# Kernel optimization log

Measured on AMD Instinct MI355X. Metric: run time of the kernel, lower is better.

Reference implementation:

```python
import jax, jax.numpy as jnp
import numpy as np
import math

B, S, E, H = 2, 2048, 1024, 8
Dh = E // H  # 128


def setup_inputs() -> dict:
    key = jax.random.key(0)
    ks = jax.random.split(key, 9)
    g = lambda k, shp: jax.random.normal(k, shp, jnp.float32) * 0.02
    return {
        "inputs": jax.random.normal(ks[0], (B, S, E), jnp.float32),
        "ln_gamma": jnp.ones((E,), jnp.float32),
        "ln_beta": jnp.zeros((E,), jnp.float32),
        "Wq": g(ks[1], (Dh, Dh)), "bq": jnp.zeros((Dh,), jnp.float32),
        "Wk": g(ks[2], (Dh, Dh)), "bk": jnp.zeros((Dh,), jnp.float32),
        "Wv": g(ks[3], (Dh, Dh)), "bv": jnp.zeros((Dh,), jnp.float32),
        "Wp": g(ks[4], (Dh, Dh)),  # pos_proj has no bias
        "u_bias": g(ks[5], (H, Dh)),
        "v_bias": g(ks[6], (H, Dh)),
        "Wo": g(ks[7], (E, E)), "bo": jnp.zeros((E,), jnp.float32),
    }


def _pos_encoding(s, e):
    # sinusoidal PE, interleaved sin/cos as in the torch module
    pos = jnp.arange(s, dtype=jnp.float32)[:, None]
    div = jnp.exp(jnp.arange(0, e, 2, dtype=jnp.float32) * (-math.log(10000.0) / e))
    pe = jnp.zeros((s, e), jnp.float32)
    pe = pe.at[:, 0::2].set(jnp.sin(pos * div))
    pe = pe.at[:, 1::2].set(jnp.cos(pos * div))
    return pe


def _rel_shift(ps):
    # Transformer-XL relative shift: pad a zero column, reshape, drop first row
    b, h, s1, s2 = ps.shape
    padded = jnp.pad(ps, ((0, 0), (0, 0), (0, 0), (1, 0)))
    return padded.reshape(b, h, s2 + 1, s1)[:, :, 1:, :].reshape(b, h, s1, s2)


def _forward(inputs, ln_gamma, ln_beta, Wq, bq, Wk, bk, Wv, bv, Wp, u_bias, v_bias, Wo, bo):
    b, s, e = inputs.shape
    # LayerNorm (biased variance, eps=1e-5 like nn.LayerNorm)
    mu = inputs.mean(-1, keepdims=True)
    var = inputs.var(-1, keepdims=True)
    xn = (inputs - mu) / jnp.sqrt(var + 1e-5) * ln_gamma + ln_beta

    xh = xn.reshape(b, s, H, Dh)              # split heads before per-head Dh x Dh projections
    q = xh @ Wq + bq                           # (b, s, H, Dh)
    k = xh @ Wk + bk
    v = xh @ Wv + bv

    pe = _pos_encoding(s, e).reshape(s, H, Dh)  # same for every batch element
    p = pe @ Wp                                 # (s, H, Dh)

    content = jnp.einsum('bqhd,bkhd->bhqk', q + u_bias, k)
    pos_score = jnp.einsum('bqhd,khd->bhqk', q + v_bias, p)
    pos_score = _rel_shift(pos_score)
    score = (content + pos_score) / jnp.sqrt(jnp.float32(e))  # note: scales by sqrt(embed_dim), faithful to source

    attn = jax.nn.softmax(score, axis=-1)
    ctx = jnp.einsum('bhqk,bkhd->bqhd', attn, v).reshape(b, s, e)
    # dropout is identity at inference
    return ctx @ Wo + bo


def reference(inputs, ln_gamma, ln_beta, Wq, bq, Wk, bk, Wv, bv, Wp, u_bias, v_bias, Wo, bo):
    return _forward(inputs, ln_gamma, ln_beta, Wq, bq, Wk, bk, Wv, bv, Wp, u_bias, v_bias, Wo, bo)
```

## Files before the change

kernel.cpp:

```cpp
#include <hip/hip_runtime.h>
#include <hip/hip_bf16.h>

#define SDIM 2048
#define EDIM 1024

typedef __attribute__((ext_vector_type(8))) short bf16x8;
typedef __attribute__((ext_vector_type(4))) short bf16x4;
typedef __attribute__((ext_vector_type(4))) float f32x4;
typedef __hip_bfloat16 bf16;

#define MFMA(a, b, c) __builtin_amdgcn_mfma_f32_16x16x32_bf16((a), (b), (c), 0, 0, 0)

#define GLDS16(g, l)                                                      \
  __builtin_amdgcn_global_load_lds(                                       \
      (const __attribute__((address_space(1))) unsigned int*)(g),         \
      (__attribute__((address_space(3))) unsigned int*)(l), 16, 0, 0)

__device__ __forceinline__ bf16x8 ld8(const bf16* p) {
  return *(const bf16x8*)p;
}
__device__ __forceinline__ float b2f(short s) {
  union { float f; unsigned u; } v; v.u = ((unsigned)(unsigned short)s) << 16; return v.f;
}

__device__ __forceinline__ void wcast_body(const float* __restrict__ w, bf16* __restrict__ wt,
                                           int blk, int R, int C) {
  __shared__ float tile[32][33];
  int cb = C >> 5;
  int br = blk / cb, bc = blk % cb;
  int r0 = br << 5, c0 = bc << 5;
  int tr = threadIdx.x >> 5, tc = threadIdx.x & 31;
#pragma unroll
  for (int i = 0; i < 32; i += 8)
    tile[tr + i][tc] = w[(size_t)(r0 + tr + i) * C + c0 + tc];
  __syncthreads();
#pragma unroll
  for (int i = 0; i < 32; i += 8)
    wt[(size_t)(c0 + tr + i) * R + r0 + tc] = __float2bfloat16(tile[tc][tr + i]);
}

__global__ __launch_bounds__(256) void wcast_all(const float* __restrict__ wo, const float* __restrict__ w0,
                                                 const float* __restrict__ w1, const float* __restrict__ w2,
                                                 const float* __restrict__ w3, bf16* __restrict__ oo,
                                                 bf16* __restrict__ o0, bf16* __restrict__ o1,
                                                 bf16* __restrict__ o2, bf16* __restrict__ o3) {
  int blk = blockIdx.x;
  if (blk < 1024) {
    wcast_body(wo, oo, blk, 1024, 1024);
  } else {
    int which = (blk - 1024) >> 4;
    const float* w = which == 0 ? w0 : which == 1 ? w1 : which == 2 ? w2 : w3;
    bf16* o = which == 0 ? o0 : which == 1 ? o1 : which == 2 ? o2 : o3;
    wcast_body(w, o, (blk - 1024) & 15, 128, 128);
  }
}

__global__ __launch_bounds__(256) void ln_kernel(const float* __restrict__ x, const float* __restrict__ g,
                                                 const float* __restrict__ be, bf16* __restrict__ xn) {
  int tok = blockIdx.x;
  const float4 v = ((const float4*)(x + (size_t)tok * EDIM))[threadIdx.x];
  float s = v.x + v.y + v.z + v.w;
  float s2 = v.x * v.x + v.y * v.y + v.z * v.z + v.w * v.w;
#pragma unroll
  for (int o = 1; o < 64; o <<= 1) { s += __shfl_xor(s, o); s2 += __shfl_xor(s2, o); }
  __shared__ float ls[8];
  if ((threadIdx.x & 63) == 0) { ls[threadIdx.x >> 6] = s; ls[4 + (threadIdx.x >> 6)] = s2; }
  __syncthreads();
  s = ls[0] + ls[1] + ls[2] + ls[3];
  s2 = ls[4] + ls[5] + ls[6] + ls[7];
  float mu = s * (1.0f / EDIM);
  float rstd = rsqrtf(s2 * (1.0f / EDIM) - mu * mu + 1e-5f);
  int c = threadIdx.x * 4;
  const float4 gv = ((const float4*)g)[threadIdx.x];
  const float4 bv = ((const float4*)be)[threadIdx.x];
  bf16* o = xn + (size_t)tok * EDIM + c;
  o[0] = __float2bfloat16((v.x - mu) * rstd * gv.x + bv.x);
  o[1] = __float2bfloat16((v.y - mu) * rstd * gv.y + bv.y);
  o[2] = __float2bfloat16((v.z - mu) * rstd * gv.z + bv.z);
  o[3] = __float2bfloat16((v.w - mu) * rstd * gv.w + bv.w);
}

__global__ __launch_bounds__(256) void pe_kernel(bf16* __restrict__ pe) {
  int s = blockIdx.x;
  for (int i = threadIdx.x; i < EDIM / 2; i += 256) {
    float div = __expf((float)(2 * i) * (-9.210340371976184f / (float)EDIM));
    float a = (float)s * div;
    float sv, cv;
    sincosf(a, &sv, &cv);
    pe[(size_t)s * EDIM + 2 * i] = __float2bfloat16(sv);
    pe[(size_t)s * EDIM + 2 * i + 1] = __float2bfloat16(cv);
  }
}

template <int MODE>
__device__ __forceinline__ void proj_body(const bf16* __restrict__ A, const bf16* __restrict__ WT,
                                          const float* __restrict__ bias, const float* __restrict__ ubias,
                                          const float* __restrict__ vbias, bf16* __restrict__ out0,
                                          bf16* __restrict__ out1, int blk, bf16* tl) {
  const int row0 = blk * 128;
  const int lane = threadIdx.x & 63, wid = threadIdx.x >> 6;
  const int wr = (wid >> 1) * 64, wc = (wid & 1) * 64;
  const int lg = lane >> 4, lr = lane & 15;
  f32x4 acc[4][4] = {};
#pragma unroll
  for (int kf = 0; kf < 4; ++kf) {
    const int k0 = kf * 32 + lg * 8;
    bf16x8 a[4], b[4];
#pragma unroll
    for (int m = 0; m < 4; ++m) a[m] = ld8(A + (size_t)(row0 + wr + m * 16 + lr) * 128 + k0);
#pragma unroll
    for (int n = 0; n < 4; ++n) b[n] = ld8(WT + (size_t)(wc + n * 16 + lr) * 128 + k0);
#pragma unroll
    for (int m = 0; m < 4; ++m)
#pragma unroll
      for (int n = 0; n < 4; ++n) acc[m][n] = MFMA(a[m], b[n], acc[m][n]);
  }
  if constexpr (MODE == 2) {
#pragma unroll
    for (int m = 0; m < 4; ++m)
#pragma unroll
      for (int n = 0; n < 4; ++n) {
        int col = wc + n * 16 + lr;
#pragma unroll
        for (int r = 0; r < 4; ++r) {
          int lrow = wr + m * 16 + lg * 4 + r;
          tl[col * 132 + lrow] = __float2bfloat16(acc[m][n][r] + bias[col]);
        }
      }
    __syncthreads();
    int tok0 = row0 >> 3;
    int b = tok0 >> 11, s0 = tok0 & 2047;
#pragma unroll
    for (int i = 0; i < 4; ++i) {
      int pair = threadIdx.x + 256 * i;
      int h = pair >> 7, d = pair & 127;
      bf16 tmp[16];
#pragma unroll
      for (int j = 0; j < 16; ++j) tmp[j] = tl[d * 132 + j * 8 + h];
      size_t o = ((size_t)((b * 8 + h) * 128 + d)) * SDIM + s0;
      *(bf16x8*)(out0 + o) = *(bf16x8*)(&tmp[0]);
      *(bf16x8*)(out0 + o + 8) = *(bf16x8*)(&tmp[8]);
    }
  } else {
#pragma unroll
    for (int m = 0; m < 4; ++m)
#pragma unroll
      for (int n = 0; n < 4; ++n) {
        int col = wc + n * 16 + lr;
#pragma unroll
        for (int r = 0; r < 4; ++r) {
          int row = row0 + wr + m * 16 + lg * 4 + r;
          float val = acc[m][n][r];
          if constexpr (MODE == 0) {
            int h = row & 7, tok = row >> 3;
            int b = tok >> 11, s = tok & 2047;
            size_t o = ((size_t)((b * 8 + h) * SDIM + s)) * 128 + col;
            val += bias[col];
            out0[o] = __float2bfloat16((val + ubias[h * 128 + col]) * 0.03125f);
            out1[o] = __float2bfloat16((val + vbias[h * 128 + col]) * 0.03125f);
          } else if constexpr (MODE == 1) {
            int h = row & 7, tok = row >> 3;
            int b = tok >> 11, s = tok & 2047;
            out0[((size_t)((b * 8 + h) * SDIM + s)) * 128 + col] = __float2bfloat16(val + bias[col]);
          } else {
            int h = row & 7, s = row >> 3;
            out0[((size_t)(h * SDIM + s)) * 128 + col] = __float2bfloat16(val);
          }
        }
      }
  }
}

__global__ __launch_bounds__(256) void proj_all(const bf16* __restrict__ xn, const bf16* __restrict__ peb,
                                                const bf16* __restrict__ wqt, const bf16* __restrict__ wkt,
                                                const bf16* __restrict__ wvt, const bf16* __restrict__ wpt,
                                                const float* __restrict__ bq, const float* __restrict__ bk,
                                                const float* __restrict__ bv, const float* __restrict__ ub,
                                                const float* __restrict__ vbias, bf16* __restrict__ qub,
                                                bf16* __restrict__ qvb, bf16* __restrict__ kbb,
                                                bf16* __restrict__ vtb, bf16* __restrict__ pb) {
  __shared__ bf16 tl[128 * 132];
  int blk = blockIdx.x;
  if (blk < 256) proj_body<0>(xn, wqt, bq, ub, vbias, qub, qvb, blk, tl);
  else if (blk < 512) proj_body<1>(xn, wkt, bk, nullptr, nullptr, kbb, nullptr, blk - 256, tl);
  else if (blk < 768) proj_body<2>(xn, wvt, bv, nullptr, nullptr, vtb, nullptr, blk - 512, tl);
  else proj_body<3>(peb, wpt, nullptr, nullptr, nullptr, pb, nullptr, blk - 768, tl);
}

__global__ __launch_bounds__(256) void ps_kernel(const bf16* __restrict__ qv, const bf16* __restrict__ p,
                                                 bf16* __restrict__ ps) {
  const int bh = blockIdx.x & 15;
  const int t = blockIdx.x >> 4;
  const int q0 = (t >> 4) * 128, j0 = (t & 15) * 128;
  const int h = bh & 7;
  const bf16* Aq = qv + (size_t)bh * SDIM * 128;
  const bf16* Ph = p + (size_t)h * SDIM * 128;
  const int lane = threadIdx.x & 63, wid = threadIdx.x >> 6;
  const int wr = (wid >> 1) * 64, wc = (wid & 1) * 64;
  const int lg = lane >> 4, lr = lane & 15;
  f32x4 acc[4][4] = {};
#pragma unroll
  for (int kf = 0; kf < 4; ++kf) {
    const int k0 = kf * 32 + lg * 8;
    bf16x8 a[4], b[4];
#pragma unroll
    for (int m = 0; m < 4; ++m) a[m] = ld8(Aq + (size_t)(q0 + wr + m * 16 + lr) * 128 + k0);
#pragma unroll
    for (int n = 0; n < 4; ++n) b[n] = ld8(Ph + (size_t)(j0 + wc + n * 16 + lr) * 128 + k0);
#pragma unroll
    for (int m = 0; m < 4; ++m)
#pragma unroll
      for (int n = 0; n < 4; ++n) acc[m][n] = MFMA(a[m], b[n], acc[m][n]);
  }
  __shared__ bf16 tl[128 * 136];
#pragma unroll
  for (int m = 0; m < 4; ++m)
#pragma unroll
    for (int n = 0; n < 4; ++n) {
      int jl = wc + n * 16 + lr;
#pragma unroll
      for (int r = 0; r < 4; ++r) {
        int ql = wr + m * 16 + lg * 4 + r;
        tl[ql * 136 + jl] = __float2bfloat16(acc[m][n][r]);
      }
    }
  __syncthreads();
  bf16* po = ps + (size_t)bh * SDIM * SDIM + (size_t)q0 * SDIM + j0;
#pragma unroll
  for (int i = 0; i < 8; ++i) {
    int id = threadIdx.x + 256 * i;
    int row = id >> 4, seg = id & 15;
    bf16x8 v = *(const bf16x8*)(tl + row * 136 + seg * 8);
    *(bf16x8*)(po + (size_t)row * SDIM + seg * 8) = v;
  }
}

#define PSLOAD(KT, WLO, WHI)                                              \
  {                                                                       \
    _Pragma("unroll")                                                     \
    for (int nf = 0; nf < 4; ++nf) {                                      \
      const int K0 = (KT) + nf * 16 + lg * 4;                             \
      const bool a_ = (K0 + 3 <= Q);                                      \
      const bf16* wp = a_ ? (pA + K0 - padA) : (pB + K0 - padB);          \
      WLO[nf] = *(const unsigned long long*)wp;                           \
      WHI[nf] = *(const unsigned long long*)(wp + 4);                     \
    }                                                                     \
  }

#define STAGE(KT, BUF)                                                    \
  {                                                                       \
    _Pragma("unroll")                                                     \
    for (int i = 0; i < 4; ++i) {                                         \
      int rb = wid * 16 + i * 4;                                          \
      int row = rb + krow_l;                                              \
      GLDS16(Kp + (size_t)((KT) + row) * 128 + ((kc16 ^ (row & 7)) << 3), \
             &kl[BUF][rb * 128]);                                         \
    }                                                                     \
    _Pragma("unroll")                                                     \
    for (int i = 0; i < 4; ++i) {                                         \
      int rb = wid * 32 + i * 8;                                          \
      int d = rb + vrow_l;                                                \
      GLDS16(Vp + (size_t)d * SDIM + (KT) + ((vc8 ^ (d & 7)) << 3),       \
             &vl[BUF][rb * 64]);                                          \
    }                                                                     \
  }

#define TILE(KT, BUF, WLO, WHI, VMSTR)                                    \
  {                                                                       \
    asm volatile("s_waitcnt vmcnt(" VMSTR ")" ::: "memory");              \
    __builtin_amdgcn_s_barrier();                                         \
    __builtin_amdgcn_sched_barrier(0);                                    \
    const bf16* klc = &kl[BUF][0];                                        \
    const bf16* vlc = &vl[BUF][0];                                        \
    f32x4 sc[4] = {};                                                     \
    _Pragma("unroll")                                                     \
    for (int nf = 0; nf < 4; ++nf) {                                      \
      const int krow = nf * 16 + lr;                                      \
      const bf16* kr = klc + krow * 128;                                  \
      const int sw = (krow & 7) << 3;                                     \
      _Pragma("unroll")                                                   \
      for (int kf = 0; kf < 4; ++kf) {                                    \
        bf16x8 kfrag = *(const bf16x8*)(kr + (((kf * 4 + lg) << 3) ^ sw));\
        sc[nf] = MFMA(kfrag, qfr[kf], sc[nf]);                            \
      }                                                                   \
    }                                                                     \
    bf16x4 pscur[4];                                                      \
    _Pragma("unroll")                                                     \
    for (int nf = 0; nf < 4; ++nf) {                                      \
      const int K0 = (KT) + nf * 16 + lg * 4;                             \
      const bool a_ = (K0 + 3 <= Q);                                      \
      const bool bp = (K0 >= Q + 2);                                      \
      const int sh = (a_ ? padA : padB) << 4;                             \
      unsigned long long w =                                              \
          sh ? ((WLO[nf] >> sh) | (WHI[nf] << (64 - sh))) : WLO[nf];      \
      union { unsigned long long u; bf16x4 v; } cv;                       \
      cv.u = w;                                                           \
      bf16x4 pv = cv.v;                                                   \
      if (!a_ && !bp) {                                                   \
        _Pragma("unroll")                                                 \
        for (int r = 0; r < 4; ++r) {                                     \
          const int K = K0 + r;                                           \
          if (K <= Q) pv[r] = ((const short*)pA)[K];                      \
          else if (K == Q + 1) pv[r] = (short)0;                          \
        }                                                                 \
      }                                                                   \
      pscur[nf] = pv;                                                     \
    }                                                                     \
    _Pragma("unroll")                                                     \
    for (int nf = 0; nf < 4; ++nf) {                                      \
      float e0 = __expf(sc[nf][0] + b2f(pscur[nf][0]));                   \
      float e1 = __expf(sc[nf][1] + b2f(pscur[nf][1]));                   \
      float e2 = __expf(sc[nf][2] + b2f(pscur[nf][2]));                   \
      float e3 = __expf(sc[nf][3] + b2f(pscur[nf][3]));                   \
      rsum += (e0 + e1) + (e2 + e3);                                      \
      bf16 tmp[4] = {__float2bfloat16(e0), __float2bfloat16(e1),          \
                     __float2bfloat16(e2), __float2bfloat16(e3)};         \
      *(bf16x4*)(plw + lr * 72 + nf * 16 + lg * 4) = *(bf16x4*)tmp;       \
    }                                                                     \
    bf16x8 pa[2];                                                         \
    _Pragma("unroll")                                                     \
    for (int k2 = 0; k2 < 2; ++k2)                                        \
      pa[k2] = *(const bf16x8*)(plw + lr * 72 + k2 * 32 + lg * 8);        \
    _Pragma("unroll")                                                     \
    for (int nf = 0; nf < 8; ++nf) {                                      \
      const int d = nf * 16 + lr;                                         \
      const bf16* vr = vlc + d * 64;                                      \
      const int swd = (d & 7) << 3;                                       \
      _Pragma("unroll")                                                   \
      for (int k2 = 0; k2 < 2; ++k2) {                                    \
        bf16x8 vb = *(const bf16x8*)(vr + (((k2 * 4 + lg) << 3) ^ swd));  \
        cacc[nf] = MFMA(pa[k2], vb, cacc[nf]);                            \
      }                                                                   \
    }                                                                     \
    asm volatile("" ::: "memory");                                        \
    __builtin_amdgcn_s_barrier();                                         \
    __builtin_amdgcn_sched_barrier(0);                                    \
  }

__global__ __launch_bounds__(256) void attn_kernel(const bf16* __restrict__ qu, const bf16* __restrict__ kb,
                                                   const bf16* __restrict__ vt, const bf16* __restrict__ ps,
                                                   bf16* __restrict__ ctx) {
  const int bh = blockIdx.x & 15, qblk = blockIdx.x >> 4;
  const int b = bh >> 3, h = bh & 7;
  const int lane = threadIdx.x & 63, wid = threadIdx.x >> 6;
  const int lg = lane >> 4, lr = lane & 15;
  const int q0 = qblk * 64 + wid * 16;
  const bf16* Kp = kb + (size_t)bh * SDIM * 128;
  const bf16* Vp = vt + (size_t)bh * 128 * SDIM;

  const bf16* psbh = ps + (size_t)bh * SDIM * SDIM;
  const int Q = q0 + lr;
  const bf16* pA = psbh + (size_t)(Q + 1) * (SDIM - 1);
  const bf16* pB = psbh + (size_t)(Q + 1) * SDIM - Q - 2;
  const int padA = (int)(((unsigned)(Q + 1) * (SDIM - 1)) & 3);
  const int padB = (int)(((unsigned)(Q + 1) * SDIM - Q - 2) & 3);

  __shared__ bf16 kl[2][64 * 128];
  __shared__ bf16 vl[2][128 * 64];
  __shared__ bf16 pl[4][16 * 72];
  bf16* plw = &pl[wid][0];

  const int krow_l = lane >> 4, kc16 = lane & 15;
  const int vrow_l = lane >> 3, vc8 = lane & 7;

  bf16x8 qfr[4];
#pragma unroll
  for (int kf = 0; kf < 4; ++kf)
    qfr[kf] = ld8(qu + (size_t)bh * SDIM * 128 + (size_t)(q0 + lr) * 128 + kf * 32 + lg * 8);

  f32x4 cacc[8] = {};
  float rsum = 0.f;

  unsigned long long wloA[4], whiA[4], wloB[4], whiB[4];

  PSLOAD(0, wloA, whiA);
  STAGE(0, 0);
  PSLOAD(64, wloB, whiB);
  STAGE(64, 1);

  for (int kt = 0; kt < SDIM - 128; kt += 128) {
    TILE(kt, 0, wloA, whiA, "16");
    PSLOAD(kt + 128, wloA, whiA);
    STAGE(kt + 128, 0);
    TILE(kt + 64, 1, wloB, whiB, "16");
    PSLOAD(kt + 192, wloB, whiB);
    STAGE(kt + 192, 1);
  }
  TILE(SDIM - 128, 0, wloA, whiA, "16");
  TILE(SDIM - 64, 1, wloB, whiB, "0");

  rsum += __shfl_xor(rsum, 16);
  rsum += __shfl_xor(rsum, 32);
  float inv[4];
#pragma unroll
  for (int r = 0; r < 4; ++r) inv[r] = 1.0f / __shfl(rsum, lg * 4 + r);
#pragma unroll
  for (int nf = 0; nf < 8; ++nf) {
#pragma unroll
    for (int r = 0; r < 4; ++r) {
      int q = q0 + lg * 4 + r;
      int d = nf * 16 + lr;
      ctx[((size_t)(b * SDIM + q) * 8 + h) * 128 + d] = __float2bfloat16(cacc[nf][r] * inv[r]);
    }
  }
}

__global__ __launch_bounds__(256) void out_gemm(const bf16* __restrict__ A, const bf16* __restrict__ WT,
                                                const float* __restrict__ bo, float* __restrict__ out) {
  const int bm = blockIdx.x >> 3, bn = blockIdx.x & 7;
  const int lane = threadIdx.x & 63, wid = threadIdx.x >> 6;
  const int wr = (wid >> 1) * 64, wc = (wid & 1) * 64;
  const int lg = lane >> 4, lr = lane & 15;
  const int row0 = bm * 128, col0 = bn * 128;
  f32x4 acc[4][4] = {};
  for (int kf = 0; kf < 32; ++kf) {
    const int k0 = kf * 32 + lg * 8;
    bf16x8 a[4], b[4];
#pragma unroll
    for (int m = 0; m < 4; ++m) a[m] = ld8(A + (size_t)(row0 + wr + m * 16 + lr) * 1024 + k0);
#pragma unroll
    for (int n = 0; n < 4; ++n) b[n] = ld8(WT + (size_t)(col0 + wc + n * 16 + lr) * 1024 + k0);
#pragma unroll
    for (int m = 0; m < 4; ++m)
#pragma unroll
      for (int n = 0; n < 4; ++n) acc[m][n] = MFMA(a[m], b[n], acc[m][n]);
  }
#pragma unroll
  for (int m = 0; m < 4; ++m)
#pragma unroll
    for (int n = 0; n < 4; ++n) {
      int col = col0 + wc + n * 16 + lr;
#pragma unroll
      for (int r = 0; r < 4; ++r) {
        int row = row0 + wr + m * 16 + lg * 4 + r;
        out[(size_t)row * 1024 + col] = acc[m][n][r] + bo[col];
      }
    }
}

extern "C" void kernel_launch(void* const* d_in, const int* in_sizes, int n_in,
                              void* d_out, int out_size, void* d_ws, size_t ws_size,
                              hipStream_t stream) {
  (void)in_sizes; (void)n_in; (void)out_size;
  const float* x = (const float*)d_in[0];
  const float* gam = (const float*)d_in[1];
  const float* bet = (const float*)d_in[2];
  const float* Wq = (const float*)d_in[3];
  const float* bq = (const float*)d_in[4];
  const float* Wk = (const float*)d_in[5];
  const float* bk = (const float*)d_in[6];
  const float* Wv = (const float*)d_in[7];
  const float* bv = (const float*)d_in[8];
  const float* Wp = (const float*)d_in[9];
  const float* ub = (const float*)d_in[10];
  const float* vbias = (const float*)d_in[11];
  const float* Wo = (const float*)d_in[12];
  const float* bo = (const float*)d_in[13];
  float* out = (float*)d_out;

  char* w = (char*)d_ws;
  size_t off = 0;
  auto take = [&](size_t n) { void* p = w + off; off += (n + 255) & ~(size_t)255; return p; };
  bf16* xn = (bf16*)take((size_t)4096 * 1024 * 2);
  bf16* peb = (bf16*)take((size_t)2048 * 1024 * 2);
  bf16* wqt = (bf16*)take(128 * 128 * 2);
  bf16* wkt = (bf16*)take(128 * 128 * 2);
  bf16* wvt = (bf16*)take(128 * 128 * 2);
  bf16* wpt = (bf16*)take(128 * 128 * 2);
  bf16* wot = (bf16*)take((size_t)1024 * 1024 * 2);
  bf16* qub = (bf16*)take((size_t)16 * 2048 * 128 * 2);
  bf16* qvb = (bf16*)take((size_t)16 * 2048 * 128 * 2);
  bf16* kbb = (bf16*)take((size_t)16 * 2048 * 128 * 2);
  bf16* vtb = (bf16*)take((size_t)16 * 2048 * 128 * 2);
  bf16* pb = (bf16*)take((size_t)8 * 2048 * 128 * 2);
  bf16* ctx = (bf16*)take((size_t)4096 * 1024 * 2);
  bf16* psb = (bf16*)take((size_t)16 * 2048 * 2048 * 2 + 4096);
  if (off > ws_size) return;

  wcast_all<<<1088, 256, 0, stream>>>(Wo, Wq, Wk, Wv, Wp, wot, wqt, wkt, wvt, wpt);
  ln_kernel<<<4096, 256, 0, stream>>>(x, gam, bet, xn);
  pe_kernel<<<2048, 256, 0, stream>>>(peb);
  proj_all<<<896, 256, 0, stream>>>(xn, peb, wqt, wkt, wvt, wpt, bq, bk, bv, ub, vbias,
                                    qub, qvb, kbb, vtb, pb);
  ps_kernel<<<4096, 256, 0, stream>>>(qvb, pb, psb);
  attn_kernel<<<512, 256, 0, stream>>>(qub, kbb, vtb, psb, ctx);
  out_gemm<<<256, 256, 0, stream>>>(ctx, wot, bo, out);
}
```

Baseline: 220.5 us.

## Widen attention blocks to 128 queries, restructure K/V prefetch, use exp2

The attention kernel now runs 512-thread blocks covering 128 queries each, so every K/V tile staged in LDS serves twice as many queries, and each warp issues half as many staging loads. The double-buffer pipeline is rewritten so each tile starts the next tile's async K/V copy and position-score loads itself, with one waitcnt and barrier at the end of each tile. s_setprio is raised around the MFMA sections. The softmax scale is folded together with log2(e) into the projection so that a raw v_exp_f32 can replace __expf. The cost is half as many blocks in the grid and a tighter synchronisation scheme that could expose load latency.

Result: faster. 209.0 us (-5.2%).

```diff
diff --git a/kernel.cpp b/kernel.cpp
--- a/kernel.cpp
+++ b/kernel.cpp
@@ -21,6 +21,11 @@
 }
 __device__ __forceinline__ float b2f(short s) {
   union { float f; unsigned u; } v; v.u = ((unsigned)(unsigned short)s) << 16; return v.f;
+}
+__device__ __forceinline__ float fexp2(float x) {
+  float r;
+  asm("v_exp_f32 %0, %1" : "=v"(r) : "v"(x));
+  return r;
 }
 
 __device__ __forceinline__ void wcast_body(const float* __restrict__ w, bf16* __restrict__ wt,
@@ -92,6 +97,7 @@
   }
 }
 
+#define QSCALE 0.045084219879837156f
 template <int MODE>
 __device__ __forceinline__ void proj_body(const bf16* __restrict__ A, const bf16* __restrict__ WT,
                                           const float* __restrict__ bias, const float* __restrict__ ubias,
@@ -156,8 +162,8 @@
             int b = tok >> 11, s = tok & 2047;
             size_t o = ((size_t)((b * 8 + h) * SDIM + s)) * 128 + col;
             val += bias[col];
-            out0[o] = __float2bfloat16((val + ubias[h * 128 + col]) * 0.03125f);
-            out1[o] = __float2bfloat16((val + vbias[h * 128 + col]) * 0.03125f);
+            out0[o] = __float2bfloat16((val + ubias[h * 128 + col]) * QSCALE);
+            out1[o] = __float2bfloat16((val + vbias[h * 128 + col]) * QSCALE);
           } else if constexpr (MODE == 1) {
             int h = row & 7, tok = row >> 3;
             int b = tok >> 11, s = tok & 2047;
@@ -250,29 +256,28 @@
 #define STAGE(KT, BUF)                                                    \
   {                                                                       \
     _Pragma("unroll")                                                     \
-    for (int i = 0; i < 4; ++i) {                                         \
-      int rb = wid * 16 + i * 4;                                          \
+    for (int i = 0; i < 2; ++i) {                                         \
+      int rb = wid * 8 + i * 4;                                           \
       int row = rb + krow_l;                                              \
       GLDS16(Kp + (size_t)((KT) + row) * 128 + ((kc16 ^ (row & 7)) << 3), \
              &kl[BUF][rb * 128]);                                         \
     }                                                                     \
     _Pragma("unroll")                                                     \
-    for (int i = 0; i < 4; ++i) {                                         \
-      int rb = wid * 32 + i * 8;                                          \
+    for (int i = 0; i < 2; ++i) {                                         \
+      int rb = wid * 16 + i * 8;                                          \
       int d = rb + vrow_l;                                                \
       GLDS16(Vp + (size_t)d * SDIM + (KT) + ((vc8 ^ (d & 7)) << 3),       \
              &vl[BUF][rb * 64]);                                          \
     }                                                                     \
   }
 
-#define TILE(KT, BUF, WLO, WHI, VMSTR)                                    \
+#define TILE(KT, BUF, WLO, WHI, WLO2, WHI2, PREF)                         \
   {                                                                       \
-    asm volatile("s_waitcnt vmcnt(" VMSTR ")" ::: "memory");              \
-    __builtin_amdgcn_s_barrier();                                         \
-    __builtin_amdgcn_sched_barrier(0);                                    \
+    if (PREF) { STAGE((KT) + 64, BUF ^ 1); }                              \
     const bf16* klc = &kl[BUF][0];                                        \
     const bf16* vlc = &vl[BUF][0];                                        \
     f32x4 sc[4] = {};                                                     \
+    __builtin_amdgcn_s_setprio(1);                                        \
     _Pragma("unroll")                                                     \
     for (int nf = 0; nf < 4; ++nf) {                                      \
       const int krow = nf * 16 + lr;                                      \
@@ -284,6 +289,7 @@
         sc[nf] = MFMA(kfrag, qfr[kf], sc[nf]);                            \
       }                                                                   \
     }                                                                     \
+    __builtin_amdgcn_s_setprio(0);                                        \
     bf16x4 pscur[4];                                                      \
     _Pragma("unroll")                                                     \
     for (int nf = 0; nf < 4; ++nf) {                                      \
@@ -306,12 +312,13 @@
       }                                                                   \
       pscur[nf] = pv;                                                     \
     }                                                                     \
+    if (PREF) { PSLOAD((KT) + 64, WLO2, WHI2); }                          \
     _Pragma("unroll")                                                     \
     for (int nf = 0; nf < 4; ++nf) {                                      \
-      float e0 = __expf(sc[nf][0] + b2f(pscur[nf][0]));                   \
-      float e1 = __expf(sc[nf][1] + b2f(pscur[nf][1]));                   \
-      float e2 = __expf(sc[nf][2] + b2f(pscur[nf][2]));                   \
-      float e3 = __expf(sc[nf][3] + b2f(pscur[nf][3]));                   \
+      float e0 = fexp2(sc[nf][0] + b2f(pscur[nf][0]));                    \
+      float e1 = fexp2(sc[nf][1] + b2f(pscur[nf][1]));                    \
+      float e2 = fexp2(sc[nf][2] + b2f(pscur[nf][2]));                    \
+      float e3 = fexp2(sc[nf][3] + b2f(pscur[nf][3]));                    \
       rsum += (e0 + e1) + (e2 + e3);                                      \
       bf16 tmp[4] = {__float2bfloat16(e0), __float2bfloat16(e1),          \
                      __float2bfloat16(e2), __float2bfloat16(e3)};         \
@@ -321,6 +328,7 @@
     _Pragma("unroll")                                                     \
     for (int k2 = 0; k2 < 2; ++k2)                                        \
       pa[k2] = *(const bf16x8*)(plw + lr * 72 + k2 * 32 + lg * 8);        \
+    __builtin_amdgcn_s_setprio(1);                                        \
     _Pragma("unroll")                                                     \
     for (int nf = 0; nf < 8; ++nf) {                                      \
       const int d = nf * 16 + lr;                                         \
@@ -332,19 +340,19 @@
         cacc[nf] = MFMA(pa[k2], vb, cacc[nf]);                            \
       }                                                                   \
     }                                                                     \
-    asm volatile("" ::: "memory");                                        \
+    __builtin_amdgcn_s_setprio(0);                                        \
+    asm volatile("s_waitcnt vmcnt(8)" ::: "memory");                      \
     __builtin_amdgcn_s_barrier();                                         \
-    __builtin_amdgcn_sched_barrier(0);                                    \
-  }
-
-__global__ __launch_bounds__(256) void attn_kernel(const bf16* __restrict__ qu, const bf16* __restrict__ kb,
+  }
+
+__global__ __launch_bounds__(512) void attn_kernel(const bf16* __restrict__ qu, const bf16* __restrict__ kb,
                                                    const bf16* __restrict__ vt, const bf16* __restrict__ ps,
                                                    bf16* __restrict__ ctx) {
   const int bh = blockIdx.x & 15, qblk = blockIdx.x >> 4;
   const int b = bh >> 3, h = bh & 7;
   const int lane = threadIdx.x & 63, wid = threadIdx.x >> 6;
   const int lg = lane >> 4, lr = lane & 15;
-  const int q0 = qblk * 64 + wid * 16;
+  const int q0 = qblk * 128 + wid * 16;
   const bf16* Kp = kb + (size_t)bh * SDIM * 128;
   const bf16* Vp = vt + (size_t)bh * 128 * SDIM;
 
@@ -357,7 +365,7 @@
 
   __shared__ bf16 kl[2][64 * 128];
   __shared__ bf16 vl[2][128 * 64];
-  __shared__ bf16 pl[4][16 * 72];
+  __shared__ bf16 pl[8][16 * 72];
   bf16* plw = &pl[wid][0];
 
   const int krow_l = lane >> 4, kc16 = lane & 15;
@@ -373,21 +381,16 @@
 
   unsigned long long wloA[4], whiA[4], wloB[4], whiB[4];
 
+  STAGE(0, 0);
   PSLOAD(0, wloA, whiA);
-  STAGE(0, 0);
-  PSLOAD(64, wloB, whiB);
-  STAGE(64, 1);
-
-  for (int kt = 0; kt < SDIM - 128; kt += 128) {
-    TILE(kt, 0, wloA, whiA, "16");
-    PSLOAD(kt + 128, wloA, whiA);
-    STAGE(kt + 128, 0);
-    TILE(kt + 64, 1, wloB, whiB, "16");
-    PSLOAD(kt + 192, wloB, whiB);
-    STAGE(kt + 192, 1);
-  }
-  TILE(SDIM - 128, 0, wloA, whiA, "16");
-  TILE(SDIM - 64, 1, wloB, whiB, "0");
+  asm volatile("s_waitcnt vmcnt(8)" ::: "memory");
+  __builtin_amdgcn_s_barrier();
+
+  for (int t2 = 0; t2 < 32; t2 += 2) {
+    const int kt = t2 * 64;
+    TILE(kt, 0, wloA, whiA, wloB, whiB, true);
+    TILE(kt + 64, 1, wloB, whiB, wloA, whiA, (t2 + 2 < 32));
+  }
 
   rsum += __shfl_xor(rsum, 16);
   rsum += __shfl_xor(rsum, 32);
@@ -483,6 +486,6 @@
   proj_all<<<896, 256, 0, stream>>>(xn, peb, wqt, wkt, wvt, wpt, bq, bk, bv, ub, vbias,
                                     qub, qvb, kbb, vtb, pb);
   ps_kernel<<<4096, 256, 0, stream>>>(qvb, pb, psb);
-  attn_kernel<<<512, 256, 0, stream>>>(qub, kbb, vtb, psb, ctx);
+  attn_kernel<<<256, 512, 0, stream>>>(qub, kbb, vtb, psb, ctx);
   out_gemm<<<256, 256, 0, stream>>>(ctx, wot, bo, out);
 }
```
